# Optimization experiments

Hardware: AMD Instinct MI355X
Metric: run time of the kernel (lower is better)

Reference implementation:

```python
import jax, jax.numpy as jnp
import numpy as np

EMB_DIM = 1024
SEQ = 2048
BATCH = 4


def setup_inputs() -> dict:
    key = jax.random.key(0)
    k1, k2, k3, k4, k5 = jax.random.split(key, 5)
    Q = jax.random.normal(k1, (SEQ, BATCH, EMB_DIM), dtype=jnp.float32)
    K = jax.random.normal(k2, (SEQ, BATCH, EMB_DIM), dtype=jnp.float32)
    V = jax.random.normal(k3, (SEQ, BATCH, EMB_DIM), dtype=jnp.float32)
    # nn.Linear default init scale ~ 1/sqrt(fan_in)
    W_in = jax.random.normal(k4, (3 * EMB_DIM, EMB_DIM), dtype=jnp.float32) / np.sqrt(EMB_DIM)
    W_out = jax.random.normal(k5, (EMB_DIM, EMB_DIM), dtype=jnp.float32) / np.sqrt(EMB_DIM)
    return {"Q": Q, "K": K, "V": V, "W_in": W_in, "W_out": W_out}


def reference(Q, K, V, W_in, W_out):
    # NOTE: original module ignores K and V args entirely (self-attention on Q).
    emb = Q.shape[-1]
    scale = 1.0 / np.sqrt(emb)
    qkv = jnp.einsum('sbe,fe->sbf', Q, W_in)        # [S, B, 3E]
    q, k, v = jnp.split(qkv, 3, axis=-1)            # each [S, B, E]
    q = jnp.transpose(q, (1, 0, 2)) * scale         # [B, S, E]
    k = jnp.transpose(k, (1, 0, 2))                 # [B, S, E]
    v = jnp.transpose(v, (1, 0, 2))                 # [B, S, E]
    scores = jnp.einsum('bte,bse->bts', q, k)       # [B, T, S]
    # per-target-row softmax over source dim == vectorized softmax on last axis
    weights = jax.nn.softmax(scores, axis=-1)       # [B, T, S]
    out = jnp.einsum('bts,bse->bte', weights, v)    # [B, T, E]
    out = jnp.transpose(out, (1, 0, 2))             # [T, B, E]
    out = jnp.einsum('tbe,fe->tbf', out, W_out)     # [T, B, E]
    return (out, weights)
```

## Files before the change

### kernel.cpp

```cpp
#include <hip/hip_runtime.h>
#include <stdint.h>

typedef unsigned short u16;
typedef __bf16 bf16_t;
typedef bf16_t bf16x8 __attribute__((ext_vector_type(8)));
typedef float f32x4 __attribute__((ext_vector_type(4)));
typedef u16 u16x4 __attribute__((ext_vector_type(4)));
typedef u16 u16x8 __attribute__((ext_vector_type(8)));

#define AS1 __attribute__((address_space(1)))
#define AS3 __attribute__((address_space(3)))

__device__ __forceinline__ u16 f2bf(float f) {
  union { float f; uint32_t u; } x; x.f = f;
  uint32_t u = x.u;
  return (u16)((u + 0x7fffu + ((u >> 16) & 1u)) >> 16);
}

__device__ __forceinline__ float bf2f(u16 b) {
  union { uint32_t u; float f; } x; x.u = ((uint32_t)b) << 16;
  return x.f;
}

__device__ __forceinline__ void gload_lds16(const void* g, void* lds) {
  __builtin_amdgcn_global_load_lds((const AS1 uint32_t*)g, (AS3 uint32_t*)lds, 16, 0, 0);
}

__global__ __launch_bounds__(256) void cvt_bf16(const float* __restrict__ in,
                                                u16* __restrict__ out, int n4) {
  int i = blockIdx.x * 256 + threadIdx.x;
  if (i >= n4) return;
  float4 v = ((const float4*)in)[i];
  u16x4 o = {f2bf(v.x), f2bf(v.y), f2bf(v.z), f2bf(v.w)};
  *(u16x4*)(out + (size_t)i * 4) = o;
}

#define BARRIER() do { asm volatile("" ::: "memory"); \
                       __builtin_amdgcn_s_barrier();  \
                       asm volatile("" ::: "memory"); } while (0)

#define MQS(MQi, NQi, ASET, BSET)                                              \
  do {                                                                         \
    __builtin_amdgcn_s_setprio(1);                                             \
    _Pragma("unroll") for (int j_ = 0; j_ < 4; ++j_) {                         \
      _Pragma("unroll") for (int i_ = 0; i_ < 2; ++i_) {                       \
        acc[(MQi) * 4 + j_][(NQi) * 2 + i_] =                                  \
            __builtin_amdgcn_mfma_f32_16x16x32_bf16(                           \
                ASET[j_][0], BSET[i_][0],                                      \
                acc[(MQi) * 4 + j_][(NQi) * 2 + i_], 0, 0, 0);                 \
        acc[(MQi) * 4 + j_][(NQi) * 2 + i_] =                                  \
            __builtin_amdgcn_mfma_f32_16x16x32_bf16(                           \
                ASET[j_][1], BSET[i_][1],                                      \
                acc[(MQi) * 4 + j_][(NQi) * 2 + i_], 0, 0, 0);                 \
      }                                                                        \
    }                                                                          \
    __builtin_amdgcn_s_setprio(0);                                             \
  } while (0)

template <bool BF16OUT>
__global__ __launch_bounds__(512, 2)
void gemm256(const u16* __restrict__ A, const u16* __restrict__ B,
             void* __restrict__ Cv,
             int lda, int ldb, int ldc,
             long long sAz, long long sBz, long long sCz,
             int K, float alpha) {
  __shared__ u16 As[2][256 * 64];
  __shared__ u16 Bs[2][256 * 64];
  const int tid  = threadIdx.x;
  const int lane = tid & 63;
  const int wid  = tid >> 6;
  const int wr   = wid >> 2;
  const int wc   = wid & 3;
  const long long z = blockIdx.z;
  const u16* Ab = A + z * sAz;
  const u16* Bb = B + z * sBz;
  const int rowBase = blockIdx.y * 256;
  const int colBase = blockIdx.x * 256;
  const int nt = K >> 6;

  const int sRow   = tid >> 3;
  const int sChunk = (tid & 7) ^ (sRow & 7);
  const size_t ldaS = (size_t)lda, ldbS = (size_t)ldb;
  const u16* aS = Ab + (size_t)(rowBase + sRow) * ldaS + sChunk * 8;
  const u16* bS = Bb + (size_t)(colBase + sRow) * ldbS + sChunk * 8;

  const int fr = lane & 15;
  const int kx = lane >> 4;
  const int rx = lane & 7;

  f32x4 acc[8][4];
  const f32x4 zf = {0.f, 0.f, 0.f, 0.f};
#pragma unroll
  for (int m = 0; m < 8; ++m)
#pragma unroll
    for (int n = 0; n < 4; ++n) acc[m][n] = zf;

  bf16x8 Ara[4][2], Arb[4][2], Bra[2][2], Brb[2][2];

  auto stageA = [&](int buf, int h, int kt) {
    const u16* s = aS + (size_t)(h * 128) * ldaS + kt;
    char* d = ((char*)&As[buf][0]) + h * 16384 + tid * 16;
    gload_lds16(s, d);
    gload_lds16(s + 64 * ldaS, d + 8192);
  };
  auto stageB = [&](int buf, int h, int kt) {
    const u16* s = bS + (size_t)(h * 128) * ldbS + kt;
    char* d = ((char*)&Bs[buf][0]) + h * 16384 + tid * 16;
    gload_lds16(s, d);
    gload_lds16(s + 64 * ldbS, d + 8192);
  };
  auto ldsA = [&](int buf, int mq, bf16x8 (&dst)[4][2]) {
#pragma unroll
    for (int j = 0; j < 4; ++j) {
      const int row = mq * 128 + wr * 64 + j * 16 + fr;
#pragma unroll
      for (int k = 0; k < 2; ++k) {
        const int ch = ((k * 4 + kx) ^ rx) * 8;
        dst[j][k] = *(const bf16x8*)&As[buf][row * 64 + ch];
      }
    }
  };
  auto ldsB = [&](int buf, int nq, bf16x8 (&dst)[2][2]) {
#pragma unroll
    for (int i = 0; i < 2; ++i) {
      const int row = nq * 128 + i * 64 + wc * 16 + fr;
#pragma unroll
      for (int k = 0; k < 2; ++k) {
        const int ch = ((k * 4 + kx) ^ rx) * 8;
        dst[i][k] = *(const bf16x8*)&Bs[buf][row * 64 + ch];
      }
    }
  };

  stageA(0, 0, 0);
  stageA(0, 1, 0);
  stageB(0, 0, 0);
  stageB(0, 1, 0);
  asm volatile("s_waitcnt vmcnt(0)" ::: "memory");
  BARRIER();
  ldsA(0, 0, Ara);
  ldsB(0, 0, Bra);

  for (int t = 0; t < nt; ++t) {
    const int c = t & 1;
    const int kt1 = (t + 1) << 6;
    const bool s1 = (t + 1 < nt);
    ldsB(c, 1, Brb);
    ldsA(c, 1, Arb);
    if (s1) {
      stageA(1 - c, 0, kt1);
      stageA(1 - c, 1, kt1);
      stageB(1 - c, 0, kt1);
      stageB(1 - c, 1, kt1);
    }
    MQS(0, 0, Ara, Bra);
    MQS(0, 1, Ara, Brb);
    if (s1) {
      asm volatile("s_waitcnt lgkmcnt(0)" ::: "memory");
      asm volatile("s_waitcnt vmcnt(0)" ::: "memory");
      BARRIER();
      ldsA(1 - c, 0, Ara);
      __builtin_amdgcn_sched_barrier(0);
    }
    MQS(1, 0, Arb, Bra);
    if (s1) ldsB(1 - c, 0, Bra);
    MQS(1, 1, Arb, Brb);
  }

  const int r0 = (lane >> 4) * 4;
#pragma unroll
  for (int m = 0; m < 8; ++m) {
    const int grow = rowBase + (m >> 2) * 128 + wr * 64 + (m & 3) * 16 + r0;
#pragma unroll
    for (int jj = 0; jj < 4; ++jj) {
      const size_t rOff = (size_t)(grow + jj) * (size_t)ldc;
      if constexpr (BF16OUT) {
        u16* C = (u16*)Cv + z * sCz;
#pragma unroll
        for (int n = 0; n < 4; ++n) {
          const int gcol = colBase + (n >> 1) * 128 + (n & 1) * 64 + wc * 16 + fr;
          C[rOff + gcol] = f2bf(acc[m][n][jj] * alpha);
        }
      } else {
        float* C = (float*)Cv + z * sCz;
#pragma unroll
        for (int n = 0; n < 4; ++n) {
          const int gcol = colBase + (n >> 1) * 128 + (n & 1) * 64 + wc * 16 + fr;
          C[rOff + gcol] = acc[m][n][jj] * alpha;
        }
      }
    }
  }
}

__global__ __launch_bounds__(256)
void transpose_v(const u16* __restrict__ qkv, u16* __restrict__ vT) {
  __shared__ u16 tile[64][72];
  const int b  = blockIdx.z;
  const int t0 = blockIdx.x * 64;
  const int e0 = blockIdx.y * 64;
  const int tid = threadIdx.x;
  const int r  = tid >> 3;
  const int c8 = (tid & 7) * 8;
#pragma unroll
  for (int p = 0; p < 2; ++p) {
    const int t = t0 + p * 32 + r;
    const u16* src = qkv + (size_t)(t * 4 + b) * 3072 + 2048 + e0 + c8;
    *(u16x8*)&tile[p * 32 + r][c8] = *(const u16x8*)src;
  }
  __syncthreads();
#pragma unroll
  for (int p = 0; p < 2; ++p) {
    const int e = p * 32 + r;
    u16x8 v;
#pragma unroll
    for (int j = 0; j < 8; ++j) v[j] = tile[c8 + j][e];
    *(u16x8*)(vT + (size_t)b * 2097152 + (size_t)(e0 + e) * 2048 + t0 + c8) = v;
  }
}

__global__ __launch_bounds__(256)
void softmax_rows(u16* __restrict__ sbf, float* __restrict__ wfp) {
  const size_t row = blockIdx.x;
  const int tid = threadIdx.x;
  u16* pb = sbf + row * 2048;
  u16x8 xb = *(const u16x8*)(pb + tid * 8);
  float x[8];
#pragma unroll
  for (int j = 0; j < 8; ++j) x[j] = bf2f(xb[j]);
  float m = x[0];
#pragma unroll
  for (int j = 1; j < 8; ++j) m = fmaxf(m, x[j]);
#pragma unroll
  for (int o = 32; o; o >>= 1) m = fmaxf(m, __shfl_xor(m, o, 64));
  __shared__ float red[8];
  if ((tid & 63) == 0) red[tid >> 6] = m;
  __syncthreads();
  m = fmaxf(fmaxf(red[0], red[1]), fmaxf(red[2], red[3]));
  float e[8];
  float s = 0.f;
#pragma unroll
  for (int j = 0; j < 8; ++j) { e[j] = expf(x[j] - m); s += e[j]; }
#pragma unroll
  for (int o = 32; o; o >>= 1) s += __shfl_xor(s, o, 64);
  if ((tid & 63) == 0) red[4 + (tid >> 6)] = s;
  __syncthreads();
  s = (red[4] + red[5]) + (red[6] + red[7]);
  const float inv = 1.0f / s;
  float w[8];
#pragma unroll
  for (int j = 0; j < 8; ++j) w[j] = e[j] * inv;
  float* pf = wfp + row * 2048;
  float4 o0 = {w[0], w[1], w[2], w[3]};
  float4 o1 = {w[4], w[5], w[6], w[7]};
  ((float4*)pf)[tid * 2] = o0;
  ((float4*)pf)[tid * 2 + 1] = o1;
  u16x8 ub;
#pragma unroll
  for (int j = 0; j < 8; ++j) ub[j] = f2bf(w[j]);
  *(u16x8*)(pb + tid * 8) = ub;
}

extern "C" void kernel_launch(void* const* d_in, const int* in_sizes, int n_in,
                              void* d_out, int out_size, void* d_ws, size_t ws_size,
                              hipStream_t stream) {
  const float* Q  = (const float*)d_in[0];
  const float* Wi = (const float*)d_in[3];
  const float* Wo = (const float*)d_in[4];
  float* out0    = (float*)d_out;
  float* weights = out0 + (size_t)2048 * 4 * 1024;

  char* ws = (char*)d_ws;
  u16* Qb   = (u16*)(ws);
  u16* Wib  = (u16*)(ws + ((size_t)16 << 20));
  u16* Wob  = (u16*)(ws + ((size_t)22 << 20));
  u16* qkvb = (u16*)(ws + ((size_t)24 << 20));
  u16* vT   = (u16*)(ws + ((size_t)72 << 20));
  u16* wbf  = (u16*)(ws + ((size_t)88 << 20));
  u16* attb = Qb;

  cvt_bf16<<<dim3(8192), dim3(256), 0, stream>>>(Q,  Qb,  2097152);
  cvt_bf16<<<dim3(3072), dim3(256), 0, stream>>>(Wi, Wib, 786432);
  cvt_bf16<<<dim3(1024), dim3(256), 0, stream>>>(Wo, Wob, 262144);

  gemm256<true><<<dim3(12, 32, 1), dim3(512), 0, stream>>>(
      Qb, Wib, (void*)qkvb, 1024, 1024, 3072, 0, 0, 0, 1024, 1.0f);

  transpose_v<<<dim3(32, 16, 4), dim3(256), 0, stream>>>(qkvb, vT);

  gemm256<true><<<dim3(8, 8, 4), dim3(512), 0, stream>>>(
      qkvb, qkvb + 1024, (void*)wbf, 12288, 12288, 2048,
      3072LL, 3072LL, 4194304LL, 1024, 0.03125f);

  softmax_rows<<<dim3(8192), dim3(256), 0, stream>>>(wbf, weights);

  gemm256<true><<<dim3(4, 8, 4), dim3(512), 0, stream>>>(
      wbf, vT, (void*)attb, 2048, 2048, 4096,
      4194304LL, 2097152LL, 1024LL, 2048, 1.0f);

  gemm256<false><<<dim3(4, 32, 1), dim3(512), 0, stream>>>(
      attb, Wob, (void*)out0, 1024, 1024, 1024, 0, 0, 0, 1024, 1.0f);
}
```

Measured before the change: 230.6 us.

## Triple-buffer A tiles in LDS with two-stage-ahead prefetch in GEMM

Grows the A shared-memory tile buffer from two stages to three and prefetches the A tile two k-steps ahead, while B stays double-buffered one step ahead. The per-iteration wait changes from a full vmcnt(0) drain to vmcnt(4), so the most recent A loads can stay in flight across the barrier. This is meant to hide global-load latency behind the MFMA work. In exchange it raises LDS use to about 160KB per block, which likely caps occupancy, and it drops the explicit lgkmcnt wait before the barrier.

Measured after the change: 248.4 us. +7.7%, slower.

```diff
diff --git a/kernel.cpp b/kernel.cpp
--- a/kernel.cpp
+++ b/kernel.cpp
@@ -64,7 +64,7 @@
              int lda, int ldb, int ldc,
              long long sAz, long long sBz, long long sCz,
              int K, float alpha) {
-  __shared__ u16 As[2][256 * 64];
+  __shared__ u16 As[3][256 * 64];
   __shared__ u16 Bs[2][256 * 64];
   const int tid  = threadIdx.x;
   const int lane = tid & 63;
@@ -136,35 +136,54 @@
   stageA(0, 1, 0);
   stageB(0, 0, 0);
   stageB(0, 1, 0);
-  asm volatile("s_waitcnt vmcnt(0)" ::: "memory");
+  if (nt > 1) {
+    stageA(1, 0, 64);
+    stageA(1, 1, 64);
+    asm volatile("s_waitcnt vmcnt(4)" ::: "memory");
+  } else {
+    asm volatile("s_waitcnt vmcnt(0)" ::: "memory");
+  }
+  __builtin_amdgcn_sched_barrier(0);
   BARRIER();
   ldsA(0, 0, Ara);
   ldsB(0, 0, Bra);
 
+  int cA = 0;
   for (int t = 0; t < nt; ++t) {
-    const int c = t & 1;
+    const int cB = t & 1;
+    int nA1 = cA + 1; if (nA1 == 3) nA1 = 0;
+    int nA2 = nA1 + 1; if (nA2 == 3) nA2 = 0;
     const int kt1 = (t + 1) << 6;
+    const int kt2 = (t + 2) << 6;
     const bool s1 = (t + 1 < nt);
-    ldsB(c, 1, Brb);
-    ldsA(c, 1, Arb);
+    const bool s2 = (t + 2 < nt);
+    ldsB(cB, 1, Brb);
+    ldsA(cA, 1, Arb);
     if (s1) {
-      stageA(1 - c, 0, kt1);
-      stageA(1 - c, 1, kt1);
-      stageB(1 - c, 0, kt1);
-      stageB(1 - c, 1, kt1);
+      stageB(1 - cB, 0, kt1);
+      stageB(1 - cB, 1, kt1);
+    }
+    if (s2) {
+      stageA(nA2, 0, kt2);
+      stageA(nA2, 1, kt2);
     }
     MQS(0, 0, Ara, Bra);
     MQS(0, 1, Ara, Brb);
     if (s1) {
-      asm volatile("s_waitcnt lgkmcnt(0)" ::: "memory");
-      asm volatile("s_waitcnt vmcnt(0)" ::: "memory");
+      if (t == nt - 2) {
+        asm volatile("s_waitcnt vmcnt(0)" ::: "memory");
+      } else {
+        asm volatile("s_waitcnt vmcnt(4)" ::: "memory");
+      }
+      __builtin_amdgcn_sched_barrier(0);
       BARRIER();
-      ldsA(1 - c, 0, Ara);
+      ldsA(nA1, 0, Ara);
       __builtin_amdgcn_sched_barrier(0);
     }
     MQS(1, 0, Arb, Bra);
-    if (s1) ldsB(1 - c, 0, Bra);
+    if (s1) ldsB(1 - cB, 0, Bra);
     MQS(1, 1, Arb, Brb);
+    cA = nA1;
   }
 
   const int r0 = (lane >> 4) * 4;
```
